# Kernel tuning notes

Measured on AMD Instinct MI355X. Metric: run time of the kernel, lower is better.

Reference implementation:

```python
import jax, jax.numpy as jnp
import numpy as np

DIM = 1024
DIM_HEAD = 64
HEADS = 16
INNER = DIM_HEAD * HEADS  # 1024
B, N1, N2 = 8, 4096, 256
EPS = 1e-5


def layer_norm(x, w, b):
    mu = jnp.mean(x, axis=-1, keepdims=True)
    var = jnp.var(x, axis=-1, keepdims=True)
    return (x - mu) * jax.lax.rsqrt(var + EPS) * w + b


def setup_inputs() -> dict:
    key = jax.random.key(0)
    ks = jax.random.split(key, 10)
    return {
        "x": jax.random.normal(ks[0], (B, N1, DIM), jnp.float32),
        "latents": jax.random.normal(ks[1], (B, N2, DIM), jnp.float32),
        "shift": jax.random.normal(ks[2], (B, DIM), jnp.float32),
        "scale": jax.random.normal(ks[3], (B, DIM), jnp.float32),
        "ln1_w": jnp.ones((DIM,), jnp.float32),
        "ln1_b": jnp.zeros((DIM,), jnp.float32),
        "ln2_w": jnp.ones((DIM,), jnp.float32),
        "ln2_b": jnp.zeros((DIM,), jnp.float32),
        "Wq": jax.random.normal(ks[4], (INNER, DIM), jnp.float32) * 0.02,
        "Wkv": jax.random.normal(ks[5], (2 * INNER, DIM), jnp.float32) * 0.02,
        "Wo": jax.random.normal(ks[6], (DIM, INNER), jnp.float32) * 0.02,
    }


def reference(x, latents, shift, scale, ln1_w, ln1_b, ln2_w, ln2_b, Wq, Wkv, Wo):
    x = layer_norm(x, ln1_w, ln1_b)                      # (b, n1, D)
    lat = layer_norm(latents, ln2_w, ln2_b)              # (b, n2, D)
    lat = lat * (1.0 + scale[:, None, :]) + shift[:, None, :]

    b, n2, _ = lat.shape
    q = jnp.einsum('bld,ed->ble', lat, Wq)               # (b, n2, inner)
    kv_in = jnp.concatenate((x, lat), axis=-2)           # (b, n1+n2, D)
    kv = jnp.einsum('bld,ed->ble', kv_in, Wkv)           # (b, n1+n2, 2*inner)
    k, v = jnp.split(kv, 2, axis=-1)

    def to_heads(t):
        bsz, L, _ = t.shape
        return t.reshape(bsz, L, HEADS, DIM_HEAD).transpose(0, 2, 1, 3)

    q, k, v = to_heads(q), to_heads(k), to_heads(v)      # (b, h, L, dh)
    attn_scale = 1.0 / np.sqrt(np.sqrt(DIM_HEAD)).astype(np.float32)
    logits = jnp.einsum('bhqd,bhkd->bhqk', q * attn_scale, k * attn_scale)
    w = jax.nn.softmax(logits.astype(jnp.float32), axis=-1).astype(logits.dtype)
    out = jnp.einsum('bhqk,bhkd->bhqd', w, v)            # (b, h, n2, dh)
    out = out.transpose(0, 2, 1, 3).reshape(b, n2, INNER)
    return jnp.einsum('ble,de->bld', out, Wo)            # (b, n2, D)
```

## Files before the change

### kernel.cpp

```cpp
#include <hip/hip_runtime.h>
#include <cstdint>
#include <cstddef>

#define B_SZ 8
#define N1 4096
#define N2 256
#define LTOT 4352
#define DIMD 1024
#define HEADS 16
#define DH 64
#define MKV (B_SZ * LTOT)

typedef _Float16 f16;
typedef f16 f16x4_t __attribute__((ext_vector_type(4)));
typedef f16 f16x8_t __attribute__((ext_vector_type(8)));
typedef float f32x4_t __attribute__((ext_vector_type(4)));

__device__ __forceinline__ void g2l16(const void* g, void* l) {
  __builtin_amdgcn_global_load_lds(
      (__attribute__((address_space(1))) void*)g,
      (__attribute__((address_space(3))) void*)l, 16, 0, 0);
}

__global__ __launch_bounds__(256) void ln_mod_kernel(
    const float* __restrict__ x, const float* __restrict__ lat,
    const float* __restrict__ shift, const float* __restrict__ scale,
    const float* __restrict__ ln1w, const float* __restrict__ ln1b,
    const float* __restrict__ ln2w, const float* __restrict__ ln2b,
    f16* __restrict__ kv_in) {
  const int row = blockIdx.x;
  const int b = row / LTOT;
  const int n = row - b * LTOT;
  const int tid = threadIdx.x;
  const bool is_lat = (n >= N1);
  const float* src = is_lat ? (lat + (size_t)(b * N2 + (n - N1)) * DIMD)
                            : (x + (size_t)(b * N1 + n) * DIMD);
  float4 v = ((const float4*)src)[tid];
  float s = v.x + v.y + v.z + v.w;
  float s2 = v.x * v.x + v.y * v.y + v.z * v.z + v.w * v.w;
#pragma unroll
  for (int m = 1; m <= 32; m <<= 1) {
    s += __shfl_xor(s, m, 64);
    s2 += __shfl_xor(s2, m, 64);
  }
  __shared__ float red[8];
  const int wave = tid >> 6;
  if ((tid & 63) == 0) { red[wave * 2] = s; red[wave * 2 + 1] = s2; }
  __syncthreads();
  s = red[0] + red[2] + red[4] + red[6];
  s2 = red[1] + red[3] + red[5] + red[7];
  const float mean = s * (1.0f / DIMD);
  const float var = fmaxf(s2 * (1.0f / DIMD) - mean * mean, 0.0f);
  const float rstd = rsqrtf(var + 1e-5f);
  const float4 w4 = ((const float4*)(is_lat ? ln2w : ln1w))[tid];
  const float4 b4 = ((const float4*)(is_lat ? ln2b : ln1b))[tid];
  float y0 = (v.x - mean) * rstd * w4.x + b4.x;
  float y1 = (v.y - mean) * rstd * w4.y + b4.y;
  float y2 = (v.z - mean) * rstd * w4.z + b4.z;
  float y3 = (v.w - mean) * rstd * w4.w + b4.w;
  if (is_lat) {
    float4 sc = ((const float4*)(scale + (size_t)b * DIMD))[tid];
    float4 sh = ((const float4*)(shift + (size_t)b * DIMD))[tid];
    y0 = y0 * (1.0f + sc.x) + sh.x;
    y1 = y1 * (1.0f + sc.y) + sh.y;
    y2 = y2 * (1.0f + sc.z) + sh.z;
    y3 = y3 * (1.0f + sc.w) + sh.w;
  }
  f16x4_t o = {(f16)y0, (f16)y1, (f16)y2, (f16)y3};
  *(f16x4_t*)(kv_in + (size_t)row * DIMD + tid * 4) = o;
}

__global__ __launch_bounds__(256) void cast_kernel(const float* __restrict__ in,
                                                   f16* __restrict__ out, int n4) {
  const int i = blockIdx.x * 256 + threadIdx.x;
  if (i < n4) {
    float4 v = ((const float4*)in)[i];
    f16x4_t o = {(f16)v.x, (f16)v.y, (f16)v.z, (f16)v.w};
    ((f16x4_t*)out)[i] = o;
  }
}

template <int MODE>
__global__ __launch_bounds__(256) void gemm128(
    const f16* __restrict__ A0, const f16* __restrict__ BT,
    void* __restrict__ out0, void* __restrict__ out1, int nt_base) {
  const int mt = blockIdx.y, nt = nt_base + blockIdx.x;
  const f16* Abase;
  if (MODE == 1) {
    const int bb = mt >> 1;
    Abase = A0 + ((size_t)(bb * LTOT + N1 + (mt & 1) * 128)) * DIMD;
  } else {
    Abase = A0 + (size_t)mt * 128 * DIMD;
  }
  const f16* Bbase = BT + (size_t)nt * 128 * DIMD;
  __shared__ alignas(16) f16 As[128 * 32];
  __shared__ alignas(16) f16 Bs[128 * 32];
  const int tid = threadIdx.x;
  const int wave = tid >> 6, lane = tid & 63;
  const int wm = (wave & 1) * 64, wn = (wave >> 1) * 64;
  const int lrow = lane >> 2, lcol = (lane & 3) * 8;
  const int r16 = lane & 15, g8 = (lane >> 4) * 8, q4 = (lane >> 4) * 4;
  f32x4_t acc[4][4] = {};
  for (int k0 = 0; k0 < DIMD; k0 += 32) {
    __syncthreads();
    g2l16(Abase + (size_t)(wave * 16 + lrow) * DIMD + k0 + lcol, &As[(wave * 16) * 32]);
    g2l16(Abase + (size_t)(64 + wave * 16 + lrow) * DIMD + k0 + lcol, &As[(64 + wave * 16) * 32]);
    g2l16(Bbase + (size_t)(wave * 16 + lrow) * DIMD + k0 + lcol, &Bs[(wave * 16) * 32]);
    g2l16(Bbase + (size_t)(64 + wave * 16 + lrow) * DIMD + k0 + lcol, &Bs[(64 + wave * 16) * 32]);
    __syncthreads();
    f16x8_t a[4], bf[4];
#pragma unroll
    for (int i = 0; i < 4; i++)
      a[i] = *(const f16x8_t*)&As[(wm + i * 16 + r16) * 32 + g8];
#pragma unroll
    for (int j = 0; j < 4; j++)
      bf[j] = *(const f16x8_t*)&Bs[(wn + j * 16 + r16) * 32 + g8];
#pragma unroll
    for (int i = 0; i < 4; i++)
#pragma unroll
      for (int j = 0; j < 4; j++)
        acc[i][j] = __builtin_amdgcn_mfma_f32_16x16x32_f16(a[i], bf[j], acc[i][j], 0, 0, 0);
  }

  if constexpr (MODE == 0) {
    const int m0 = mt * 128;
    const int b = m0 / LTOT;
    const int n0 = m0 - b * LTOT;
    const int e0 = nt * 128;
    if (e0 < 1024) {
      f16* kbuf = (f16*)out0;
#pragma unroll
      for (int i = 0; i < 4; i++) {
        const int n_base = n0 + wm + i * 16 + q4;
#pragma unroll
        for (int j = 0; j < 4; j++) {
          const int e = e0 + wn + j * 16 + r16;
          const int h = e >> 6, d = e & 63;
          const size_t base = ((size_t)(b * HEADS + h) * LTOT);
#pragma unroll
          for (int r = 0; r < 4; r++)
            kbuf[(base + n_base + r) * DH + d] = (f16)acc[i][j][r];
        }
      }
    } else {
      f16* vbuf = (f16*)out1;
      const int e0v = e0 - 1024;
#pragma unroll
      for (int i = 0; i < 4; i++) {
        const int n_base = n0 + wm + i * 16 + q4;
#pragma unroll
        for (int j = 0; j < 4; j++) {
          const int e = e0v + wn + j * 16 + r16;
          const int h = e >> 6, d = e & 63;
          f16x4_t pk = {(f16)acc[i][j][0], (f16)acc[i][j][1],
                        (f16)acc[i][j][2], (f16)acc[i][j][3]};
          *(f16x4_t*)&vbuf[((size_t)(b * HEADS + h) * DH + d) * LTOT + n_base] = pk;
        }
      }
    }
  } else if constexpr (MODE == 1) {
    f16* qbuf = (f16*)out0;
    const int b = mt >> 1;
#pragma unroll
    for (int i = 0; i < 4; i++) {
      const int n_base = (mt & 1) * 128 + wm + i * 16 + q4;
#pragma unroll
      for (int j = 0; j < 4; j++) {
        const int e = nt * 128 + wn + j * 16 + r16;
        const int h = e >> 6, d = e & 63;
#pragma unroll
        for (int r = 0; r < 4; r++)
          qbuf[((size_t)(b * HEADS + h) * N2 + n_base + r) * DH + d] = (f16)acc[i][j][r];
      }
    }
  } else {
    float* outp = (float*)out0;
    const int m0 = mt * 128;
#pragma unroll
    for (int i = 0; i < 4; i++) {
#pragma unroll
      for (int j = 0; j < 4; j++) {
        const int col = nt * 128 + wn + j * 16 + r16;
#pragma unroll
        for (int r = 0; r < 4; r++)
          outp[(size_t)(m0 + wm + i * 16 + q4 + r) * DIMD + col] = acc[i][j][r];
      }
    }
  }
}

__global__ __launch_bounds__(256, 1) void attn_kernel(
    const f16* __restrict__ qbuf, const f16* __restrict__ kbuf,
    const f16* __restrict__ vbuf, f16* __restrict__ attn_out) {
  const int bh = blockIdx.x >> 1;
  const int qt = blockIdx.x & 1;
  const int b = bh >> 4, h = bh & 15;
  const f16* qg = qbuf + ((size_t)bh * N2 + qt * 128) * DH;
  const f16* kg = kbuf + (size_t)bh * LTOT * DH;
  const f16* vg = vbuf + (size_t)bh * DH * LTOT;

  __shared__ alignas(16) f16 Rh[17408];
  __shared__ alignas(16) f16 Vs[4][64 * 32];

  const int tid = threadIdx.x, wave = tid >> 6, lane = tid & 63;
  const int lrow = lane >> 2, lcol = (lane & 3) * 8;
  const int r16 = lane & 15, g8 = (lane >> 4) * 8, q4 = (lane >> 4) * 4;
  f16* Ps = &Rh[wave * 4352];

#pragma unroll
  for (int s = 0; s < 2; s++)
#pragma unroll
    for (int half = 0; half < 2; half++) {
      const int r0 = half * 64 + wave * 16;
      g2l16(qg + (size_t)(r0 + lrow) * DH + s * 32 + lcol,
            &Rh[8192 + s * 4096 + r0 * 32]);
    }
  __syncthreads();
  f16x8_t bQ[2][2];
#pragma unroll
  for (int s = 0; s < 2; s++)
#pragma unroll
    for (int j = 0; j < 2; j++)
      bQ[s][j] = *(const f16x8_t*)&Rh[8192 + s * 4096 + (wave * 32 + j * 16 + r16) * 32 + g8];

  f32x4_t oacc[4][2] = {};
  float mrow[2] = {-1e30f, -1e30f};
  float lsum[2] = {0.0f, 0.0f};
  const float SCL = 0.125f * 1.44269504089f;

  for (int kt = 0; kt < LTOT / 128; kt++) {
    __syncthreads();
#pragma unroll
    for (int s = 0; s < 2; s++)
#pragma unroll
      for (int half = 0; half < 2; half++) {
        const int r0 = half * 64 + wave * 16;
        g2l16(kg + (size_t)(kt * 128 + r0 + lrow) * DH + s * 32 + lcol,
              &Rh[s * 4096 + r0 * 32]);
      }
#pragma unroll
    for (int dg = 0; dg < 4; dg++) {
      const int d0 = dg * 16;
      g2l16(vg + (size_t)(d0 + lrow) * LTOT + kt * 128 + wave * 32 + lcol,
            &Vs[wave][d0 * 32]);
    }
    __syncthreads();
    f32x4_t sacc[8][2] = {};
#pragma unroll
    for (int s = 0; s < 2; s++) {
      f16x8_t aK[8];
#pragma unroll
      for (int i = 0; i < 8; i++)
        aK[i] = *(const f16x8_t*)&Rh[s * 4096 + (i * 16 + r16) * 32 + g8];
#pragma unroll
      for (int i = 0; i < 8; i++)
#pragma unroll
        for (int j = 0; j < 2; j++)
          sacc[i][j] = __builtin_amdgcn_mfma_f32_16x16x32_f16(aK[i], bQ[s][j], sacc[i][j], 0, 0, 0);
    }
    __syncthreads();
#pragma unroll
    for (int j = 0; j < 2; j++) {
      float vmax = -1e30f;
#pragma unroll
      for (int i = 0; i < 8; i++)
#pragma unroll
        for (int r = 0; r < 4; r++) vmax = fmaxf(vmax, sacc[i][j][r]);
      vmax = fmaxf(vmax, __shfl_xor(vmax, 16, 64));
      vmax = fmaxf(vmax, __shfl_xor(vmax, 32, 64));
      const float m_new = fmaxf(mrow[j], SCL * vmax);
      const float alpha = exp2f(mrow[j] - m_new);
      float psum = 0.0f;
#pragma unroll
      for (int i = 0; i < 8; i++) {
        f16x4_t pk;
#pragma unroll
        for (int r = 0; r < 4; r++) {
          const float p = exp2f(SCL * sacc[i][j][r] - m_new);
          psum += p;
          pk[r] = (f16)p;
        }
        *(f16x4_t*)&Ps[(j * 16 + r16) * 136 + i * 16 + q4] = pk;
      }
      psum += __shfl_xor(psum, 16, 64);
      psum += __shfl_xor(psum, 32, 64);
      lsum[j] = lsum[j] * alpha + psum;
      mrow[j] = m_new;
#pragma unroll
      for (int id = 0; id < 4; id++) oacc[id][j] *= alpha;
    }
#pragma unroll
    for (int s2 = 0; s2 < 4; s2++) {
      f16x8_t aV[4];
#pragma unroll
      for (int id = 0; id < 4; id++)
        aV[id] = *(const f16x8_t*)&Vs[s2][(id * 16 + r16) * 32 + g8];
      f16x8_t bP[2];
#pragma unroll
      for (int j = 0; j < 2; j++)
        bP[j] = *(const f16x8_t*)&Ps[(j * 16 + r16) * 136 + s2 * 32 + g8];
#pragma unroll
      for (int id = 0; id < 4; id++)
#pragma unroll
        for (int j = 0; j < 2; j++)
          oacc[id][j] = __builtin_amdgcn_mfma_f32_16x16x32_f16(aV[id], bP[j], oacc[id][j], 0, 0, 0);
    }
  }
#pragma unroll
  for (int j = 0; j < 2; j++) {
    const float inv = 1.0f / lsum[j];
    const int qrow = qt * 128 + wave * 32 + j * 16 + r16;
    const size_t rowbase = ((size_t)(b * N2 + qrow)) * DIMD + h * DH;
#pragma unroll
    for (int id = 0; id < 4; id++) {
      f16x4_t pk;
#pragma unroll
      for (int r = 0; r < 4; r++) pk[r] = (f16)(oacc[id][j][r] * inv);
      *(f16x4_t*)&attn_out[rowbase + id * 16 + q4] = pk;
    }
  }
}

extern "C" void kernel_launch(void* const* d_in, const int* in_sizes, int n_in,
                              void* d_out, int out_size, void* d_ws, size_t ws_size,
                              hipStream_t stream) {
  const float* x     = (const float*)d_in[0];
  const float* lat   = (const float*)d_in[1];
  const float* shift = (const float*)d_in[2];
  const float* scale = (const float*)d_in[3];
  const float* ln1w  = (const float*)d_in[4];
  const float* ln1b  = (const float*)d_in[5];
  const float* ln2w  = (const float*)d_in[6];
  const float* ln2b  = (const float*)d_in[7];
  const float* Wq    = (const float*)d_in[8];
  const float* Wkv   = (const float*)d_in[9];
  const float* Wo    = (const float*)d_in[10];
  float* outp = (float*)d_out;

  char* ws = (char*)d_ws;
  f16* kv_in = (f16*)ws;                 ws += (size_t)MKV * DIMD * 2;
  f16* Wq16  = (f16*)ws;                 ws += (size_t)1024 * 1024 * 2;
  f16* Wkv16 = (f16*)ws;                 ws += (size_t)2048 * 1024 * 2;
  f16* Wo16  = (f16*)ws;                 ws += (size_t)1024 * 1024 * 2;
  f16* qbuf  = (f16*)ws;                 ws += (size_t)B_SZ * HEADS * N2 * DH * 2;
  f16* kbuf  = (f16*)ws;                 ws += (size_t)B_SZ * HEADS * LTOT * DH * 2;
  f16* vbuf  = (f16*)ws;                 ws += (size_t)B_SZ * HEADS * LTOT * DH * 2;
  f16* aout  = (f16*)ws;                 ws += (size_t)B_SZ * N2 * DIMD * 2;

  ln_mod_kernel<<<dim3(MKV), dim3(256), 0, stream>>>(x, lat, shift, scale, ln1w,
                                                     ln1b, ln2w, ln2b, kv_in);
  cast_kernel<<<dim3(1024), dim3(256), 0, stream>>>(Wq, Wq16, 1024 * 1024 / 4);
  cast_kernel<<<dim3(2048), dim3(256), 0, stream>>>(Wkv, Wkv16, 2048 * 1024 / 4);
  cast_kernel<<<dim3(1024), dim3(256), 0, stream>>>(Wo, Wo16, 1024 * 1024 / 4);

  gemm128<0><<<dim3(8, MKV / 128), dim3(256), 0, stream>>>(kv_in, Wkv16, kbuf, vbuf, 0);
  gemm128<0><<<dim3(8, MKV / 128), dim3(256), 0, stream>>>(kv_in, Wkv16, kbuf, vbuf, 8);
  gemm128<1><<<dim3(8, 16), dim3(256), 0, stream>>>(kv_in, Wq16, qbuf, nullptr, 0);
  attn_kernel<<<dim3(256), dim3(256), 0, stream>>>(qbuf, kbuf, vbuf, aout);
  gemm128<2><<<dim3(8, 16), dim3(256), 0, stream>>>(aout, Wo16, outp, nullptr, 0);
}
```

Measured before the change: 606.6 us.

## Double-buffer K/V tiles in attention with 8 waves and 64-key tiles

Rewrites the attention kernel to use 512 threads (8 waves, 16 query rows each) and 64-key tiles. K and V tiles are double-buffered in LDS, with async global-to-LDS prefetch two tiles ahead, and synchronisation uses explicit vmcnt waits plus raw barriers. The goal is to overlap K/V loads with MFMA and softmax work and to raise the number of waves per CU. The trade-off is more iterations with smaller tiles, more barriers, and fragile hand-written waitcnt accounting.

```diff
diff --git a/kernel.cpp b/kernel.cpp
--- a/kernel.cpp
+++ b/kernel.cpp
@@ -10,6 +10,8 @@
 #define HEADS 16
 #define DH 64
 #define MKV (B_SZ * LTOT)
+#define ATILE 64
+#define AITERS (LTOT / ATILE)
 
 typedef _Float16 f16;
 typedef f16 f16x4_t __attribute__((ext_vector_type(4)));
@@ -189,7 +191,7 @@
   }
 }
 
-__global__ __launch_bounds__(256, 1) void attn_kernel(
+__global__ __launch_bounds__(512, 1) void attn_kernel(
     const f16* __restrict__ qbuf, const f16* __restrict__ kbuf,
     const f16* __restrict__ vbuf, f16* __restrict__ attn_out) {
   const int bh = blockIdx.x >> 1;
@@ -199,125 +201,107 @@
   const f16* kg = kbuf + (size_t)bh * LTOT * DH;
   const f16* vg = vbuf + (size_t)bh * DH * LTOT;
 
-  __shared__ alignas(16) f16 Rh[17408];
-  __shared__ alignas(16) f16 Vs[4][64 * 32];
+  __shared__ alignas(16) f16 Ks[2][4096];
+  __shared__ alignas(16) f16 Vs[2][4096];
+  __shared__ alignas(16) f16 QP[9216];
 
   const int tid = threadIdx.x, wave = tid >> 6, lane = tid & 63;
   const int lrow = lane >> 2, lcol = (lane & 3) * 8;
   const int r16 = lane & 15, g8 = (lane >> 4) * 8, q4 = (lane >> 4) * 4;
-  f16* Ps = &Rh[wave * 4352];
-
+  f16* Ps = &QP[wave * 1152];
+
+#pragma unroll
+  for (int i = 0; i < 2; i++) {
+    const int c = wave * 2 + i, s = c >> 3, rb = (c & 7) * 16;
+    g2l16(qg + (size_t)(rb + lrow) * DH + s * 32 + lcol, &QP[s * 4096 + rb * 32]);
+  }
+  auto stage = [&](int kt, int buf) {
+    const int s = wave >> 2, rb = (wave & 3) * 16;
+    g2l16(kg + (size_t)(kt * ATILE + rb + lrow) * DH + s * 32 + lcol,
+          &Ks[buf][s * 2048 + rb * 32]);
+    g2l16(vg + (size_t)(rb + lrow) * LTOT + kt * ATILE + s * 32 + lcol,
+          &Vs[buf][s * 2048 + rb * 32]);
+  };
+  stage(0, 0);
+  stage(1, 1);
+  asm volatile("s_waitcnt vmcnt(4)" ::: "memory");
+  asm volatile("s_barrier" ::: "memory");
+  f16x8_t bQ[2];
 #pragma unroll
   for (int s = 0; s < 2; s++)
-#pragma unroll
-    for (int half = 0; half < 2; half++) {
-      const int r0 = half * 64 + wave * 16;
-      g2l16(qg + (size_t)(r0 + lrow) * DH + s * 32 + lcol,
-            &Rh[8192 + s * 4096 + r0 * 32]);
-    }
-  __syncthreads();
-  f16x8_t bQ[2][2];
-#pragma unroll
-  for (int s = 0; s < 2; s++)
-#pragma unroll
-    for (int j = 0; j < 2; j++)
-      bQ[s][j] = *(const f16x8_t*)&Rh[8192 + s * 4096 + (wave * 32 + j * 16 + r16) * 32 + g8];
-
-  f32x4_t oacc[4][2] = {};
-  float mrow[2] = {-1e30f, -1e30f};
-  float lsum[2] = {0.0f, 0.0f};
+    bQ[s] = *(const f16x8_t*)&QP[s * 4096 + (wave * 16 + r16) * 32 + g8];
+  asm volatile("s_waitcnt lgkmcnt(0)" ::: "memory");
+
+  f32x4_t oacc[4] = {};
+  float mrow = -1e30f, lsum = 0.0f;
   const float SCL = 0.125f * 1.44269504089f;
 
-  for (int kt = 0; kt < LTOT / 128; kt++) {
-    __syncthreads();
-#pragma unroll
-    for (int s = 0; s < 2; s++)
-#pragma unroll
-      for (int half = 0; half < 2; half++) {
-        const int r0 = half * 64 + wave * 16;
-        g2l16(kg + (size_t)(kt * 128 + r0 + lrow) * DH + s * 32 + lcol,
-              &Rh[s * 4096 + r0 * 32]);
-      }
-#pragma unroll
-    for (int dg = 0; dg < 4; dg++) {
-      const int d0 = dg * 16;
-      g2l16(vg + (size_t)(d0 + lrow) * LTOT + kt * 128 + wave * 32 + lcol,
-            &Vs[wave][d0 * 32]);
-    }
-    __syncthreads();
-    f32x4_t sacc[8][2] = {};
+  for (int kt = 0; kt < AITERS; kt++) {
+    const int cur = kt & 1;
+    asm volatile("s_waitcnt vmcnt(2)" ::: "memory");
+    asm volatile("s_barrier" ::: "memory");
+    f32x4_t sacc[4] = {};
 #pragma unroll
     for (int s = 0; s < 2; s++) {
-      f16x8_t aK[8];
-#pragma unroll
-      for (int i = 0; i < 8; i++)
-        aK[i] = *(const f16x8_t*)&Rh[s * 4096 + (i * 16 + r16) * 32 + g8];
-#pragma unroll
-      for (int i = 0; i < 8; i++)
-#pragma unroll
-        for (int j = 0; j < 2; j++)
-          sacc[i][j] = __builtin_amdgcn_mfma_f32_16x16x32_f16(aK[i], bQ[s][j], sacc[i][j], 0, 0, 0);
-    }
-    __syncthreads();
-#pragma unroll
-    for (int j = 0; j < 2; j++) {
-      float vmax = -1e30f;
-#pragma unroll
-      for (int i = 0; i < 8; i++)
-#pragma unroll
-        for (int r = 0; r < 4; r++) vmax = fmaxf(vmax, sacc[i][j][r]);
-      vmax = fmaxf(vmax, __shfl_xor(vmax, 16, 64));
-      vmax = fmaxf(vmax, __shfl_xor(vmax, 32, 64));
-      const float m_new = fmaxf(mrow[j], SCL * vmax);
-      const float alpha = exp2f(mrow[j] - m_new);
-      float psum = 0.0f;
-#pragma unroll
-      for (int i = 0; i < 8; i++) {
-        f16x4_t pk;
-#pragma unroll
-        for (int r = 0; r < 4; r++) {
-          const float p = exp2f(SCL * sacc[i][j][r] - m_new);
-          psum += p;
-          pk[r] = (f16)p;
-        }
-        *(f16x4_t*)&Ps[(j * 16 + r16) * 136 + i * 16 + q4] = pk;
-      }
-      psum += __shfl_xor(psum, 16, 64);
-      psum += __shfl_xor(psum, 32, 64);
-      lsum[j] = lsum[j] * alpha + psum;
-      mrow[j] = m_new;
-#pragma unroll
-      for (int id = 0; id < 4; id++) oacc[id][j] *= alpha;
-    }
-#pragma unroll
-    for (int s2 = 0; s2 < 4; s2++) {
+      f16x8_t aK[4];
+#pragma unroll
+      for (int i = 0; i < 4; i++)
+        aK[i] = *(const f16x8_t*)&Ks[cur][s * 2048 + (i * 16 + r16) * 32 + g8];
+#pragma unroll
+      for (int i = 0; i < 4; i++)
+        sacc[i] = __builtin_amdgcn_mfma_f32_16x16x32_f16(aK[i], bQ[s], sacc[i], 0, 0, 0);
+    }
+    float vmax = -1e30f;
+#pragma unroll
+    for (int i = 0; i < 4; i++)
+#pragma unroll
+      for (int r = 0; r < 4; r++) vmax = fmaxf(vmax, sacc[i][r]);
+    vmax = fmaxf(vmax, __shfl_xor(vmax, 16, 64));
+    vmax = fmaxf(vmax, __shfl_xor(vmax, 32, 64));
+    const float m_new = fmaxf(mrow, SCL * vmax);
+    const float alpha = exp2f(mrow - m_new);
+    float psum = 0.0f;
+#pragma unroll
+    for (int i = 0; i < 4; i++) {
+      f16x4_t pk;
+#pragma unroll
+      for (int r = 0; r < 4; r++) {
+        const float p = exp2f(SCL * sacc[i][r] - m_new);
+        psum += p;
+        pk[r] = (f16)p;
+      }
+      *(f16x4_t*)&Ps[r16 * 72 + i * 16 + q4] = pk;
+    }
+    psum += __shfl_xor(psum, 16, 64);
+    psum += __shfl_xor(psum, 32, 64);
+    lsum = lsum * alpha + psum;
+    mrow = m_new;
+#pragma unroll
+    for (int id = 0; id < 4; id++) oacc[id] *= alpha;
+#pragma unroll
+    for (int s2 = 0; s2 < 2; s2++) {
       f16x8_t aV[4];
 #pragma unroll
       for (int id = 0; id < 4; id++)
-        aV[id] = *(const f16x8_t*)&Vs[s2][(id * 16 + r16) * 32 + g8];
-      f16x8_t bP[2];
-#pragma unroll
-      for (int j = 0; j < 2; j++)
-        bP[j] = *(const f16x8_t*)&Ps[(j * 16 + r16) * 136 + s2 * 32 + g8];
+        aV[id] = *(const f16x8_t*)&Vs[cur][s2 * 2048 + (id * 16 + r16) * 32 + g8];
+      const f16x8_t bP = *(const f16x8_t*)&Ps[r16 * 72 + s2 * 32 + g8];
 #pragma unroll
       for (int id = 0; id < 4; id++)
-#pragma unroll
-        for (int j = 0; j < 2; j++)
-          oacc[id][j] = __builtin_amdgcn_mfma_f32_16x16x32_f16(aV[id], bP[j], oacc[id][j], 0, 0, 0);
-    }
-  }
-#pragma unroll
-  for (int j = 0; j < 2; j++) {
-    const float inv = 1.0f / lsum[j];
-    const int qrow = qt * 128 + wave * 32 + j * 16 + r16;
-    const size_t rowbase = ((size_t)(b * N2 + qrow)) * DIMD + h * DH;
-#pragma unroll
-    for (int id = 0; id < 4; id++) {
-      f16x4_t pk;
-#pragma unroll
-      for (int r = 0; r < 4; r++) pk[r] = (f16)(oacc[id][j][r] * inv);
-      *(f16x4_t*)&attn_out[rowbase + id * 16 + q4] = pk;
-    }
+        oacc[id] = __builtin_amdgcn_mfma_f32_16x16x32_f16(aV[id], bP, oacc[id], 0, 0, 0);
+    }
+    asm volatile("s_waitcnt lgkmcnt(0)" ::: "memory");
+    asm volatile("s_barrier" ::: "memory");
+    if (kt + 2 < AITERS) stage(kt + 2, cur);
+  }
+  const float inv = 1.0f / lsum;
+  const int q = qt * 128 + wave * 16 + r16;
+  const size_t rowbase = ((size_t)(b * N2 + q)) * DIMD + h * DH;
+#pragma unroll
+  for (int id = 0; id < 4; id++) {
+    f16x4_t pk;
+#pragma unroll
+    for (int r = 0; r < 4; r++) pk[r] = (f16)(oacc[id][r] * inv);
+    *(f16x4_t*)&attn_out[rowbase + id * 16 + q4] = pk;
   }
 }
 
@@ -356,6 +340,6 @@
   gemm128<0><<<dim3(8, MKV / 128), dim3(256), 0, stream>>>(kv_in, Wkv16, kbuf, vbuf, 0);
   gemm128<0><<<dim3(8, MKV / 128), dim3(256), 0, stream>>>(kv_in, Wkv16, kbuf, vbuf, 8);
   gemm128<1><<<dim3(8, 16), dim3(256), 0, stream>>>(kv_in, Wq16, qbuf, nullptr, 0);
-  attn_kernel<<<dim3(256), dim3(256), 0, stream>>>(qbuf, kbuf, vbuf, aout);
+  attn_kernel<<<dim3(256), dim3(512), 0, stream>>>(qbuf, kbuf, vbuf, aout);
   gemm128<2><<<dim3(8, 16), dim3(256), 0, stream>>>(aout, Wo16, outp, nullptr, 0);
 }
```

New measurement: 579.4 us. -4.5%, faster.
